# Optimization experiments

Hardware: AMD Instinct MI355X
Metric: run time of the kernel (lower is better)

The kernel has to match this reference:

```python
import jax, jax.numpy as jnp
import numpy as np

HEADS = 8
DIM_HEAD = 64
INNER = HEADS * DIM_HEAD  # 512
QUERY_DIM = 512
CONTEXT_DIM = 512


def setup_inputs() -> dict:
    key = jax.random.key(0)
    ks = jax.random.split(key, 10)
    s_in = 1.0 / np.sqrt(QUERY_DIM)
    s_ctx = 1.0 / np.sqrt(CONTEXT_DIM)
    s_o = 1.0 / np.sqrt(INNER)
    return {
        "x": jax.random.normal(ks[0], (8, QUERY_DIM, 32, 32), jnp.float32),
        "context": jax.random.normal(ks[1], (8, CONTEXT_DIM, 32, 32), jnp.float32),
        "Wq": jax.random.normal(ks[2], (INNER, QUERY_DIM), jnp.float32) * s_in,
        "bq": jnp.zeros((INNER,), jnp.float32),
        "Wk": jax.random.normal(ks[3], (INNER, CONTEXT_DIM), jnp.float32) * s_ctx,
        "bk": jnp.zeros((INNER,), jnp.float32),
        "Wv": jax.random.normal(ks[4], (INNER, CONTEXT_DIM), jnp.float32) * s_ctx,
        "bv": jnp.zeros((INNER,), jnp.float32),
        "Wo": jax.random.normal(ks[5], (QUERY_DIM, INNER), jnp.float32) * s_o,
        "bo": jnp.zeros((QUERY_DIM,), jnp.float32),
    }


def _proj1x1(t, W, b):
    # 1x1 Conv2d: channel mixing only. t: [B,Cin,X,Y], W: [Cout,Cin]
    return jnp.einsum('bcxy,oc->boxy', t, W) + b[None, :, None, None]


def reference(x, context, Wq, bq, Wk, bk, Wv, bv, Wo, bo):
    b, c, h, w = x.shape
    scale = DIM_HEAD ** (-0.5)

    q = _proj1x1(x, Wq, bq)
    k = _proj1x1(context, Wk, bk)
    v = _proj1x1(context, Wv, bv)

    def split_heads(t):
        B, C, X, Y = t.shape  # C = HEADS*DIM_HEAD
        return t.reshape(B, HEADS, DIM_HEAD, X * Y)  # b h d n

    q = split_heads(q) * scale
    k = split_heads(k)
    v = split_heads(v)

    sim = jnp.einsum('bhdi,bhdj->bhij', q, k)          # [b,h,i,j]
    attn = jax.nn.softmax(sim, axis=-1)
    out = jnp.einsum('bhij,bhdj->bhid', attn, v)       # [b,h,i,d]
    # rearrange 'b h (x y) d -> b (h d) x y'
    out = out.transpose(0, 1, 3, 2).reshape(b, HEADS * DIM_HEAD, h, w)
    return _proj1x1(out, Wo, bo)
```

## Files before the change

kernel.cpp:

```cpp
#include <hip/hip_runtime.h>
#include <stdint.h>

#define NB   8
#define CH   512
#define NPIX 1024
#define DH   64

typedef float  f32x4  __attribute__((ext_vector_type(4)));
typedef float  f32x16 __attribute__((ext_vector_type(16)));
typedef __bf16 bf16x8 __attribute__((ext_vector_type(8)));
typedef unsigned int u32x4 __attribute__((ext_vector_type(4)));

static __device__ __forceinline__ unsigned short f2bf(float f) {
    unsigned int u = __builtin_bit_cast(unsigned int, f);
    u += 0x7FFFu + ((u >> 16) & 1u);
    return (unsigned short)(u >> 16);
}

static __device__ __forceinline__ bf16x8 ld_bf8(const unsigned short* p) {
    return *reinterpret_cast<const bf16x8*>(p);
}

static __device__ __forceinline__ unsigned int cvtpk_bf16(float lo, float hi) {
    unsigned int r;
    asm("v_cvt_pk_bf16_f32 %0,%1,%2" : "=v"(r) : "v"(lo), "v"(hi));
    return r;
}

static __device__ __forceinline__ float fexp2(float x) {
    float r;
    asm("v_exp_f32 %0, %1" : "=v"(r) : "v"(x));
    return r;
}

static __device__ __forceinline__ void plswap(unsigned int& a, unsigned int& b) {
    asm("v_permlane32_swap_b32 %0, %1" : "+v"(a), "+v"(b));
}

static __device__ __forceinline__ void glds16(const unsigned short* g, void* l) {
    __builtin_amdgcn_global_load_lds(
        (const __attribute__((address_space(1))) unsigned int*)g,
        (__attribute__((address_space(3))) unsigned int*)l,
        16, 0, 0);
}

#define WAIT_VMCNT_8() asm volatile("s_waitcnt vmcnt(8)" ::: "memory")
#define WAIT_VMCNT_4() asm volatile("s_waitcnt vmcnt(4)" ::: "memory")
#define WAIT_VMCNT_0() asm volatile("s_waitcnt vmcnt(0)" ::: "memory")
#define WAIT_LGKM_0()  asm volatile("s_waitcnt lgkmcnt(0)" ::: "memory")

__global__ __launch_bounds__(256) void prep_kernel(
        const float* __restrict__ Wq, const float* __restrict__ Wk,
        const float* __restrict__ Wv, const float* __restrict__ Wo,
        unsigned short* __restrict__ Wbf,
        const float* __restrict__ x, const float* __restrict__ ctx,
        unsigned short* __restrict__ XT, unsigned short* __restrict__ CT) {
    __shared__ float tile[32][33];
    const int bid = blockIdx.x;
    if (bid < 1024) {
        int idx4 = (bid * 256 + threadIdx.x) * 4;
        int which = idx4 >> 18;
        int off   = idx4 & 0x3FFFF;
        const float* src = which == 0 ? Wq : which == 1 ? Wk : which == 2 ? Wv : Wo;
        float4 v = *(const float4*)(src + off);
        unsigned int lo = ((unsigned)f2bf(v.y) << 16) | f2bf(v.x);
        unsigned int hi = ((unsigned)f2bf(v.w) << 16) | f2bf(v.z);
        *(uint2*)(Wbf + idx4) = make_uint2(lo, hi);
        return;
    }
    const int t0 = bid - 1024;
    const int z  = t0 >> 9;
    const int cx = t0 & 15, ny = (t0 >> 4) & 31;
    const float* src = (z < 8) ? x : ctx;
    unsigned short* dst = (z < 8) ? XT : CT;
    const int b  = z & 7;
    const int c0 = cx * 32, n0 = ny * 32;
    const int t  = threadIdx.x;
    const int r  = t >> 3, ch4 = (t & 7) * 4;
    const float* s = src + (size_t)b * CH * NPIX + (size_t)(c0 + r) * NPIX + n0 + ch4;
    float4 v4 = *(const float4*)s;
    tile[r][ch4] = v4.x; tile[r][ch4 + 1] = v4.y;
    tile[r][ch4 + 2] = v4.z; tile[r][ch4 + 3] = v4.w;
    __syncthreads();
    unsigned int lo = ((unsigned)f2bf(tile[ch4 + 1][r]) << 16) | f2bf(tile[ch4][r]);
    unsigned int hw = ((unsigned)f2bf(tile[ch4 + 3][r]) << 16) | f2bf(tile[ch4 + 2][r]);
    *(uint2*)(dst + (size_t)b * NPIX * CH + (size_t)(n0 + r) * CH + c0 + ch4)
        = make_uint2(lo, hw);
}

static __device__ __forceinline__ void gemm128(
        const unsigned short* __restrict__ Wp,
        const unsigned short* __restrict__ Xp,
        f32x4 acc[4][4]) {
    __shared__ __align__(16) unsigned short lA[3][128][32];
    __shared__ __align__(16) unsigned short lB[3][128][32];
    const int tid  = threadIdx.x;
    const int lane = tid & 63;
    const int wv   = tid >> 6;
    const int wm   = wv & 1, wn = tid >> 7;

    const unsigned short* gA = Wp + (size_t)(wv * 32 + (lane >> 2)) * CH + (lane & 3) * 8;
    const unsigned short* gB = Xp + (size_t)(wv * 32 + (lane >> 2)) * CH + (lane & 3) * 8;

    auto stage = [&](int kt, int buf) {
        const int k0 = kt * 32;
        char* dA = (char*)&lA[buf][0][0] + wv * 2048;
        char* dB = (char*)&lB[buf][0][0] + wv * 2048;
        glds16(gA + k0,           dA);
        glds16(gA + k0 + 16 * CH, dA + 1024);
        glds16(gB + k0,           dB);
        glds16(gB + k0 + 16 * CH, dB + 1024);
    };

    stage(0, 0);
    stage(1, 1);

#pragma unroll 1
    for (int kt = 0; kt < 16; kt++) {
        if (kt < 15) { WAIT_VMCNT_4(); } else { WAIT_VMCNT_0(); }
        __builtin_amdgcn_s_barrier();
        if (kt + 2 < 16) stage(kt + 2, (kt + 2) % 3);
        const int buf = kt % 3;
        bf16x8 af[4], bfrag[4];
#pragma unroll
        for (int i = 0; i < 4; i++)
            af[i] = ld_bf8(&lA[buf][wm * 64 + i * 16 + (lane & 15)][(lane >> 4) * 8]);
#pragma unroll
        for (int j = 0; j < 4; j++)
            bfrag[j] = ld_bf8(&lB[buf][wn * 64 + j * 16 + (lane & 15)][(lane >> 4) * 8]);
#pragma unroll
        for (int i = 0; i < 4; i++)
#pragma unroll
            for (int j = 0; j < 4; j++)
                acc[i][j] = __builtin_amdgcn_mfma_f32_16x16x32_bf16(af[i], bfrag[j], acc[i][j], 0, 0, 0);
    }
}

__global__ __launch_bounds__(256) void proj_qkv_kernel(
        const unsigned short* __restrict__ XT, const unsigned short* __restrict__ CT,
        const unsigned short* __restrict__ Wbf,
        const float* __restrict__ bq, const float* __restrict__ bk, const float* __restrict__ bv,
        unsigned short* __restrict__ Q, unsigned short* __restrict__ K, unsigned short* __restrict__ V) {
    const int id = blockIdx.x;
    const int b = id & 7, mode = id >> 8, inner = (id >> 3) & 31;
    const int o0 = (inner & 3) * 128, n0 = (inner >> 2) * 128;
    const unsigned short* W = Wbf + (size_t)mode * CH * CH;
    const unsigned short* X = (mode == 0 ? XT : CT) + (size_t)b * NPIX * CH;
    const float* bias = mode == 0 ? bq : mode == 1 ? bk : bv;

    f32x4 acc[4][4];
#pragma unroll
    for (int i = 0; i < 4; i++)
#pragma unroll
        for (int j = 0; j < 4; j++)
#pragma unroll
            for (int r = 0; r < 4; r++) acc[i][j][r] = 0.f;

    gemm128(W + (size_t)o0 * CH, X + (size_t)n0 * CH, acc);

    const int lane = threadIdx.x & 63;
    const int wm = (threadIdx.x >> 6) & 1, wn = threadIdx.x >> 7;
    const float qs = 0.125f * 1.44269504088896340736f;
#pragma unroll
    for (int i = 0; i < 4; i++) {
        const int ob = o0 + wm * 64 + i * 16 + (lane >> 4) * 4;
        const int h = ob >> 6, dd = ob & 63;
        float b4[4];
#pragma unroll
        for (int r = 0; r < 4; r++) b4[r] = bias[ob + r];
#pragma unroll
        for (int j = 0; j < 4; j++) {
            const int n = n0 + wn * 64 + j * 16 + (lane & 15);
            float v[4];
#pragma unroll
            for (int r = 0; r < 4; r++) v[r] = acc[i][j][r] + b4[r];
            if (mode == 0) {
#pragma unroll
                for (int r = 0; r < 4; r++) v[r] *= qs;
            }
            if (mode <= 1) {
                unsigned int lo = (unsigned)f2bf(v[0]) | ((unsigned)f2bf(v[1]) << 16);
                unsigned int hi = (unsigned)f2bf(v[2]) | ((unsigned)f2bf(v[3]) << 16);
                unsigned short* dst = (mode == 0 ? Q : K) +
                    (((size_t)(b * 8 + h) * NPIX) + n) * DH + dd;
                *(uint2*)dst = make_uint2(lo, hi);
            } else {
#pragma unroll
                for (int r = 0; r < 4; r++) {
                    int d = dd + r;
                    V[(((size_t)(b * 8 + h) * 32 + (n >> 5)) * 2048)
                      + (size_t)(d & 31) * 64 + (d >> 5) * 32 + (n & 31)] = f2bf(v[r]);
                }
            }
        }
    }
}

__global__ __launch_bounds__(128) void attn_kernel(
        const unsigned short* __restrict__ Qg, const unsigned short* __restrict__ Kg,
        const unsigned short* __restrict__ Vg, unsigned short* __restrict__ AT) {
    __shared__ __align__(16) unsigned short ldsS[2][2][2][2048];
    __shared__ float lbuf[64];

    const int p  = blockIdx.x;
    const int local = p >> 3;
    const int bh = ((p & 7) << 3) | (local >> 4);
    const int qb = local & 15;
    const int q0 = qb * 64;
    const int tid = threadIdx.x, wave = tid >> 6, lane = tid & 63;
    const int lq = lane & 31, hi = lane >> 5, lql7 = lq & 7;
    const int key0 = wave * 512;

    const unsigned short* Qp = Qg + ((size_t)bh * NPIX + q0 + lq) * DH + hi * 8;
    bf16x8 qa[4], qbf[4];
#pragma unroll
    for (int ds = 0; ds < 4; ds++) {
        qa[ds]  = ld_bf8(Qp + ds * 16);
        qbf[ds] = ld_bf8(Qp + 32 * DH + ds * 16);
    }

    f32x16 oA0, oA1, oB0, oB1, zro;
#pragma unroll
    for (int r = 0; r < 16; r++) {
        oA0[r] = 0.f; oA1[r] = 0.f; oB0[r] = 0.f; oB1[r] = 0.f; zro[r] = 0.f;
    }
    float lA = 0.f, lB = 0.f;

    const int swz = (((lane & 7) ^ ((lane >> 3) & 7)) << 3);
    const unsigned short* gK = Kg + ((size_t)bh * NPIX + key0 + (lane >> 3)) * DH + swz;
    const unsigned short* gV = Vg + (size_t)bh * 65536 + (size_t)(key0 >> 5) * 2048
                                  + (lane >> 3) * 64 + swz;

    auto stage = [&](int t, int buf) {
        const unsigned short* sk = gK + (size_t)t * 32 * DH;
        char* dK = (char*)&ldsS[wave][buf][0][0];
        glds16(sk,           dK);
        glds16(sk +  8 * DH, dK + 1024);
        glds16(sk + 16 * DH, dK + 2048);
        glds16(sk + 24 * DH, dK + 3072);
        const unsigned short* sv = gV + (size_t)t * 2048;
        char* dV = (char*)&ldsS[wave][buf][1][0];
        glds16(sv,        dV);
        glds16(sv +  512, dV + 1024);
        glds16(sv + 1024, dV + 2048);
        glds16(sv + 1536, dV + 3072);
    };

    stage(0, 0);
    stage(1, 1);

#pragma unroll 1
    for (int t = 0; t < 16; ++t) {
        if (t < 15) { WAIT_VMCNT_8(); } else { WAIT_VMCNT_0(); }
        const int cur = t & 1;
        const unsigned short* kb = &ldsS[wave][cur][0][0] + lq * 64;
        bf16x8 kf0 = ld_bf8(kb + (((0 + hi) ^ lql7) << 3));
        bf16x8 kf1 = ld_bf8(kb + (((2 + hi) ^ lql7) << 3));
        bf16x8 kf2 = ld_bf8(kb + (((4 + hi) ^ lql7) << 3));
        bf16x8 kf3 = ld_bf8(kb + (((6 + hi) ^ lql7) << 3));
        const unsigned short* vb = &ldsS[wave][cur][1][0] + lq * 64;
        bf16x8 v00 = ld_bf8(vb + (((0 + hi) ^ lql7) << 3));
        bf16x8 v01 = ld_bf8(vb + (((2 + hi) ^ lql7) << 3));
        bf16x8 v10 = ld_bf8(vb + (((4 + hi) ^ lql7) << 3));
        bf16x8 v11 = ld_bf8(vb + (((6 + hi) ^ lql7) << 3));

        f32x16 sA, sB;
        __builtin_amdgcn_s_setprio(1);
        sA = __builtin_amdgcn_mfma_f32_32x32x16_bf16(kf0, qa[0],  zro, 0, 0, 0);
        sA = __builtin_amdgcn_mfma_f32_32x32x16_bf16(kf1, qa[1],  sA, 0, 0, 0);
        sA = __builtin_amdgcn_mfma_f32_32x32x16_bf16(kf2, qa[2],  sA, 0, 0, 0);
        sA = __builtin_amdgcn_mfma_f32_32x32x16_bf16(kf3, qa[3],  sA, 0, 0, 0);
        sB = __builtin_amdgcn_mfma_f32_32x32x16_bf16(kf0, qbf[0], zro, 0, 0, 0);
        sB = __builtin_amdgcn_mfma_f32_32x32x16_bf16(kf1, qbf[1], sB, 0, 0, 0);
        sB = __builtin_amdgcn_mfma_f32_32x32x16_bf16(kf2, qbf[2], sB, 0, 0, 0);
        sB = __builtin_amdgcn_mfma_f32_32x32x16_bf16(kf3, qbf[3], sB, 0, 0, 0);
        __builtin_amdgcn_s_setprio(0);

        WAIT_LGKM_0();
        __builtin_amdgcn_sched_barrier(0);
        if (t + 2 < 16) stage(t + 2, cur);
        __builtin_amdgcn_sched_barrier(0);

#pragma unroll
        for (int r = 0; r < 16; r++) sA[r] = fexp2(sA[r]);
        {
            float a8[8], a4[4];
#pragma unroll
            for (int i = 0; i < 8; i++) a8[i] = sA[2*i] + sA[2*i+1];
#pragma unroll
            for (int i = 0; i < 4; i++) a4[i] = a8[2*i] + a8[2*i+1];
            lA += (a4[0] + a4[1]) + (a4[2] + a4[3]);
        }
        bf16x8 paA[2];
#pragma unroll
        for (int ks = 0; ks < 2; ks++) {
            const int bse = ks * 8;
            unsigned int X0 = cvtpk_bf16(sA[bse + 0], sA[bse + 1]);
            unsigned int X1 = cvtpk_bf16(sA[bse + 2], sA[bse + 3]);
            unsigned int X2 = cvtpk_bf16(sA[bse + 4], sA[bse + 5]);
            unsigned int X3 = cvtpk_bf16(sA[bse + 6], sA[bse + 7]);
            plswap(X0, X2); plswap(X1, X3);
            u32x4 wa; wa[0] = X0; wa[1] = X1; wa[2] = X2; wa[3] = X3;
            paA[ks] = __builtin_bit_cast(bf16x8, wa);
        }

        __builtin_amdgcn_s_setprio(1);
        oA0 = __builtin_amdgcn_mfma_f32_32x32x16_bf16(paA[0], v00, oA0, 0, 0, 0);
        oA1 = __builtin_amdgcn_mfma_f32_32x32x16_bf16(paA[0], v10, oA1, 0, 0, 0);
        oA0 = __builtin_amdgcn_mfma_f32_32x32x16_bf16(paA[1], v01, oA0, 0, 0, 0);
        oA1 = __builtin_amdgcn_mfma_f32_32x32x16_bf16(paA[1], v11, oA1, 0, 0, 0);
        __builtin_amdgcn_s_setprio(0);

#pragma unroll
        for (int r = 0; r < 16; r++) sB[r] = fexp2(sB[r]);
        {
            float b8[8], b4[4];
#pragma unroll
            for (int i = 0; i < 8; i++) b8[i] = sB[2*i] + sB[2*i+1];
#pragma unroll
            for (int i = 0; i < 4; i++) b4[i] = b8[2*i] + b8[2*i+1];
            lB += (b4[0] + b4[1]) + (b4[2] + b4[3]);
        }
        bf16x8 paB[2];
#pragma unroll
        for (int ks = 0; ks < 2; ks++) {
            const int bse = ks * 8;
            unsigned int Y0 = cvtpk_bf16(sB[bse + 0], sB[bse + 1]);
            unsigned int Y1 = cvtpk_bf16(sB[bse + 2], sB[bse + 3]);
            unsigned int Y2 = cvtpk_bf16(sB[bse + 4], sB[bse + 5]);
            unsigned int Y3 = cvtpk_bf16(sB[bse + 6], sB[bse + 7]);
            plswap(Y0, Y2); plswap(Y1, Y3);
            u32x4 wb; wb[0] = Y0; wb[1] = Y1; wb[2] = Y2; wb[3] = Y3;
            paB[ks] = __builtin_bit_cast(bf16x8, wb);
        }

        __builtin_amdgcn_s_setprio(1);
        oB0 = __builtin_amdgcn_mfma_f32_32x32x16_bf16(paB[0], v00, oB0, 0, 0, 0);
        oB1 = __builtin_amdgcn_mfma_f32_32x32x16_bf16(paB[0], v10, oB1, 0, 0, 0);
        oB0 = __builtin_amdgcn_mfma_f32_32x32x16_bf16(paB[1], v01, oB0, 0, 0, 0);
        oB1 = __builtin_amdgcn_mfma_f32_32x32x16_bf16(paB[1], v11, oB1, 0, 0, 0);
        __builtin_amdgcn_s_setprio(0);
    }

    lA += __shfl_xor(lA, 32);
    lB += __shfl_xor(lB, 32);
    float* obuf = (float*)&ldsS[1][0][0][0];
    if (wave == 1) {
#pragma unroll
        for (int r = 0; r < 16; r++) {
            obuf[(0 * 16 + r) * 64 + lane] = oA0[r];
            obuf[(1 * 16 + r) * 64 + lane] = oA1[r];
            obuf[(2 * 16 + r) * 64 + lane] = oB0[r];
            obuf[(3 * 16 + r) * 64 + lane] = oB1[r];
        }
        if (lane < 32) { lbuf[lq] = lA; lbuf[32 + lq] = lB; }
    }
    __syncthreads();
    if (wave == 0) {
        float invA = 1.0f / (lA + lbuf[lq]);
        float invB = 1.0f / (lB + lbuf[32 + lq]);
        const int b = bh >> 3, h = bh & 7;
#pragma unroll
        for (int r = 0; r < 16; r++) {
            float a0 = oA0[r] + obuf[(0 * 16 + r) * 64 + lane];
            float a1 = oA1[r] + obuf[(1 * 16 + r) * 64 + lane];
            float b0 = oB0[r] + obuf[(2 * 16 + r) * 64 + lane];
            float b1 = oB1[r] + obuf[(3 * 16 + r) * 64 + lane];
            int crow = (r & 3) + 8 * (r >> 2) + 4 * hi;
            float facA = __shfl(invA, crow);
            float facB = __shfl(invB, crow);
            unsigned short* dA = AT + ((size_t)b * NPIX + q0 + crow) * CH + h * 64 + lq;
            dA[0]  = f2bf(a0 * facA);
            dA[32] = f2bf(a1 * facA);
            unsigned short* dB = AT + ((size_t)b * NPIX + q0 + 32 + crow) * CH + h * 64 + lq;
            dB[0]  = f2bf(b0 * facB);
            dB[32] = f2bf(b1 * facB);
        }
    }
}

__global__ __launch_bounds__(256) void proj_out_kernel(
        const unsigned short* __restrict__ AT, const unsigned short* __restrict__ Wo,
        const float* __restrict__ bo, float* __restrict__ out) {
    const int id = blockIdx.x;
    const int b = id & 7, inner = id >> 3;
    const int o0 = (inner & 3) * 128, n0 = (inner >> 2) * 128;
    f32x4 acc[4][4];
#pragma unroll
    for (int i = 0; i < 4; i++)
#pragma unroll
        for (int j = 0; j < 4; j++)
#pragma unroll
            for (int r = 0; r < 4; r++) acc[i][j][r] = 0.f;

    gemm128(Wo + (size_t)o0 * CH, AT + ((size_t)b * NPIX + n0) * CH, acc);

    const int lane = threadIdx.x & 63;
    const int wm = (threadIdx.x >> 6) & 1, wn = threadIdx.x >> 7;
#pragma unroll
    for (int i = 0; i < 4; i++) {
        const int ob = o0 + wm * 64 + i * 16 + (lane >> 4) * 4;
        float b4[4];
#pragma unroll
        for (int r = 0; r < 4; r++) b4[r] = bo[ob + r];
#pragma unroll
        for (int j = 0; j < 4; j++) {
            const int n = n0 + wn * 64 + j * 16 + (lane & 15);
#pragma unroll
            for (int r = 0; r < 4; r++)
                out[((size_t)b * CH + ob + r) * NPIX + n] = acc[i][j][r] + b4[r];
        }
    }
}

extern "C" void kernel_launch(void* const* d_in, const int* in_sizes, int n_in,
                              void* d_out, int out_size, void* d_ws, size_t ws_size,
                              hipStream_t stream) {
    const float* x   = (const float*)d_in[0];
    const float* ctx = (const float*)d_in[1];
    const float* Wq  = (const float*)d_in[2];
    const float* bq  = (const float*)d_in[3];
    const float* Wk  = (const float*)d_in[4];
    const float* bk  = (const float*)d_in[5];
    const float* Wv  = (const float*)d_in[6];
    const float* bv  = (const float*)d_in[7];
    const float* Wo  = (const float*)d_in[8];
    const float* bo  = (const float*)d_in[9];
    float* out = (float*)d_out;

    char* ws = (char*)d_ws;
    unsigned short* XT  = (unsigned short*)(ws);
    unsigned short* CT  = (unsigned short*)(ws + 8388608);
    unsigned short* Wbf = (unsigned short*)(ws + 16777216);
    unsigned short* Q   = (unsigned short*)(ws + 18874368);
    unsigned short* K   = (unsigned short*)(ws + 27262976);
    unsigned short* V   = (unsigned short*)(ws + 35651584);
    unsigned short* AT  = XT;

    prep_kernel<<<9216, 256, 0, stream>>>(Wq, Wk, Wv, Wo, Wbf, x, ctx, XT, CT);
    proj_qkv_kernel<<<768, 256, 0, stream>>>(XT, CT, Wbf, bq, bk, bv, Q, K, V);
    attn_kernel<<<1024, 128, 0, stream>>>(Q, K, V, AT);
    proj_out_kernel<<<256, 256, 0, stream>>>(AT, Wbf + 3 * 262144, bo, out);
}
```

Measured before the change: 82.42 us.

## Software-pipeline QK^T of next tile with softmax and PV of current tile

Moves the QK^T MFMAs for tile t+1 ahead of the PV MFMAs for tile t, with a prologue computing tile 0's scores before the loop. The exp and convert work for both A and B halves is merged into one block, and the PV MFMAs are interleaved A/B so independent accumulator chains overlap. The aim is to hide VALU exp latency and MFMA dependency stalls behind independent matrix work. It raises register pressure by keeping sA/sB live across iterations, and it changes the buffer-reuse and wait ordering, so overwrites of the K/V staging buffers need care.

```diff
diff --git a/kernel.cpp b/kernel.cpp
--- a/kernel.cpp
+++ b/kernel.cpp
@@ -249,22 +249,14 @@
     stage(0, 0);
     stage(1, 1);
 
-#pragma unroll 1
-    for (int t = 0; t < 16; ++t) {
-        if (t < 15) { WAIT_VMCNT_8(); } else { WAIT_VMCNT_0(); }
-        const int cur = t & 1;
-        const unsigned short* kb = &ldsS[wave][cur][0][0] + lq * 64;
+    f32x16 sA, sB;
+    {
+        WAIT_VMCNT_8();
+        const unsigned short* kb = &ldsS[wave][0][0][0] + lq * 64;
         bf16x8 kf0 = ld_bf8(kb + (((0 + hi) ^ lql7) << 3));
         bf16x8 kf1 = ld_bf8(kb + (((2 + hi) ^ lql7) << 3));
         bf16x8 kf2 = ld_bf8(kb + (((4 + hi) ^ lql7) << 3));
         bf16x8 kf3 = ld_bf8(kb + (((6 + hi) ^ lql7) << 3));
-        const unsigned short* vb = &ldsS[wave][cur][1][0] + lq * 64;
-        bf16x8 v00 = ld_bf8(vb + (((0 + hi) ^ lql7) << 3));
-        bf16x8 v01 = ld_bf8(vb + (((2 + hi) ^ lql7) << 3));
-        bf16x8 v10 = ld_bf8(vb + (((4 + hi) ^ lql7) << 3));
-        bf16x8 v11 = ld_bf8(vb + (((6 + hi) ^ lql7) << 3));
-
-        f32x16 sA, sB;
         __builtin_amdgcn_s_setprio(1);
         sA = __builtin_amdgcn_mfma_f32_32x32x16_bf16(kf0, qa[0],  zro, 0, 0, 0);
         sA = __builtin_amdgcn_mfma_f32_32x32x16_bf16(kf1, qa[1],  sA, 0, 0, 0);
@@ -275,23 +267,29 @@
         sB = __builtin_amdgcn_mfma_f32_32x32x16_bf16(kf2, qbf[2], sB, 0, 0, 0);
         sB = __builtin_amdgcn_mfma_f32_32x32x16_bf16(kf3, qbf[3], sB, 0, 0, 0);
         __builtin_amdgcn_s_setprio(0);
-
-        WAIT_LGKM_0();
-        __builtin_amdgcn_sched_barrier(0);
-        if (t + 2 < 16) stage(t + 2, cur);
-        __builtin_amdgcn_sched_barrier(0);
-
-#pragma unroll
-        for (int r = 0; r < 16; r++) sA[r] = fexp2(sA[r]);
+    }
+
+#pragma unroll 1
+    for (int t = 0; t < 16; ++t) {
+        const int cur = t & 1;
+        const unsigned short* vb = &ldsS[wave][cur][1][0] + lq * 64;
+        bf16x8 v00 = ld_bf8(vb + (((0 + hi) ^ lql7) << 3));
+        bf16x8 v01 = ld_bf8(vb + (((2 + hi) ^ lql7) << 3));
+        bf16x8 v10 = ld_bf8(vb + (((4 + hi) ^ lql7) << 3));
+        bf16x8 v11 = ld_bf8(vb + (((6 + hi) ^ lql7) << 3));
+
+#pragma unroll
+        for (int r = 0; r < 16; r++) { sA[r] = fexp2(sA[r]); sB[r] = fexp2(sB[r]); }
         {
-            float a8[8], a4[4];
-#pragma unroll
-            for (int i = 0; i < 8; i++) a8[i] = sA[2*i] + sA[2*i+1];
-#pragma unroll
-            for (int i = 0; i < 4; i++) a4[i] = a8[2*i] + a8[2*i+1];
+            float a8[8], b8[8], a4[4], b4[4];
+#pragma unroll
+            for (int i = 0; i < 8; i++) { a8[i] = sA[2*i] + sA[2*i+1]; b8[i] = sB[2*i] + sB[2*i+1]; }
+#pragma unroll
+            for (int i = 0; i < 4; i++) { a4[i] = a8[2*i] + a8[2*i+1]; b4[i] = b8[2*i] + b8[2*i+1]; }
             lA += (a4[0] + a4[1]) + (a4[2] + a4[3]);
-        }
-        bf16x8 paA[2];
+            lB += (b4[0] + b4[1]) + (b4[2] + b4[3]);
+        }
+        bf16x8 paA[2], paB[2];
 #pragma unroll
         for (int ks = 0; ks < 2; ks++) {
             const int bse = ks * 8;
@@ -302,29 +300,6 @@
             plswap(X0, X2); plswap(X1, X3);
             u32x4 wa; wa[0] = X0; wa[1] = X1; wa[2] = X2; wa[3] = X3;
             paA[ks] = __builtin_bit_cast(bf16x8, wa);
-        }
-
-        __builtin_amdgcn_s_setprio(1);
-        oA0 = __builtin_amdgcn_mfma_f32_32x32x16_bf16(paA[0], v00, oA0, 0, 0, 0);
-        oA1 = __builtin_amdgcn_mfma_f32_32x32x16_bf16(paA[0], v10, oA1, 0, 0, 0);
-        oA0 = __builtin_amdgcn_mfma_f32_32x32x16_bf16(paA[1], v01, oA0, 0, 0, 0);
-        oA1 = __builtin_amdgcn_mfma_f32_32x32x16_bf16(paA[1], v11, oA1, 0, 0, 0);
-        __builtin_amdgcn_s_setprio(0);
-
-#pragma unroll
-        for (int r = 0; r < 16; r++) sB[r] = fexp2(sB[r]);
-        {
-            float b8[8], b4[4];
-#pragma unroll
-            for (int i = 0; i < 8; i++) b8[i] = sB[2*i] + sB[2*i+1];
-#pragma unroll
-            for (int i = 0; i < 4; i++) b4[i] = b8[2*i] + b8[2*i+1];
-            lB += (b4[0] + b4[1]) + (b4[2] + b4[3]);
-        }
-        bf16x8 paB[2];
-#pragma unroll
-        for (int ks = 0; ks < 2; ks++) {
-            const int bse = ks * 8;
             unsigned int Y0 = cvtpk_bf16(sB[bse + 0], sB[bse + 1]);
             unsigned int Y1 = cvtpk_bf16(sB[bse + 2], sB[bse + 3]);
             unsigned int Y2 = cvtpk_bf16(sB[bse + 4], sB[bse + 5]);
@@ -334,10 +309,38 @@
             paB[ks] = __builtin_bit_cast(bf16x8, wb);
         }
 
+        WAIT_LGKM_0();
+        __builtin_amdgcn_sched_barrier(0);
+        if (t + 2 < 16) stage(t + 2, cur);
+        __builtin_amdgcn_sched_barrier(0);
+
+        if (t < 15) {
+            if (t < 14) { WAIT_VMCNT_8(); } else { WAIT_VMCNT_0(); }
+            const unsigned short* kb = &ldsS[wave][cur ^ 1][0][0] + lq * 64;
+            bf16x8 kf0 = ld_bf8(kb + (((0 + hi) ^ lql7) << 3));
+            bf16x8 kf1 = ld_bf8(kb + (((2 + hi) ^ lql7) << 3));
+            bf16x8 kf2 = ld_bf8(kb + (((4 + hi) ^ lql7) << 3));
+            bf16x8 kf3 = ld_bf8(kb + (((6 + hi) ^ lql7) << 3));
+            __builtin_amdgcn_s_setprio(1);
+            sA = __builtin_amdgcn_mfma_f32_32x32x16_bf16(kf0, qa[0],  zro, 0, 0, 0);
+            sA = __builtin_amdgcn_mfma_f32_32x32x16_bf16(kf1, qa[1],  sA, 0, 0, 0);
+            sA = __builtin_amdgcn_mfma_f32_32x32x16_bf16(kf2, qa[2],  sA, 0, 0, 0);
+            sA = __builtin_amdgcn_mfma_f32_32x32x16_bf16(kf3, qa[3],  sA, 0, 0, 0);
+            sB = __builtin_amdgcn_mfma_f32_32x32x16_bf16(kf0, qbf[0], zro, 0, 0, 0);
+            sB = __builtin_amdgcn_mfma_f32_32x32x16_bf16(kf1, qbf[1], sB, 0, 0, 0);
+            sB = __builtin_amdgcn_mfma_f32_32x32x16_bf16(kf2, qbf[2], sB, 0, 0, 0);
+            sB = __builtin_amdgcn_mfma_f32_32x32x16_bf16(kf3, qbf[3], sB, 0, 0, 0);
+            __builtin_amdgcn_s_setprio(0);
+        }
+
         __builtin_amdgcn_s_setprio(1);
+        oA0 = __builtin_amdgcn_mfma_f32_32x32x16_bf16(paA[0], v00, oA0, 0, 0, 0);
         oB0 = __builtin_amdgcn_mfma_f32_32x32x16_bf16(paB[0], v00, oB0, 0, 0, 0);
+        oA1 = __builtin_amdgcn_mfma_f32_32x32x16_bf16(paA[0], v10, oA1, 0, 0, 0);
         oB1 = __builtin_amdgcn_mfma_f32_32x32x16_bf16(paB[0], v10, oB1, 0, 0, 0);
+        oA0 = __builtin_amdgcn_mfma_f32_32x32x16_bf16(paA[1], v01, oA0, 0, 0, 0);
         oB0 = __builtin_amdgcn_mfma_f32_32x32x16_bf16(paB[1], v01, oB0, 0, 0, 0);
+        oA1 = __builtin_amdgcn_mfma_f32_32x32x16_bf16(paA[1], v11, oA1, 0, 0, 0);
         oB1 = __builtin_amdgcn_mfma_f32_32x32x16_bf16(paB[1], v11, oB1, 0, 0, 0);
         __builtin_amdgcn_s_setprio(0);
     }
```

New measurement: 80.93 us. About the same (-1.8%).
